# Kernel tuning notes

Measured on AMD Instinct MI355X. Metric: run time of the kernel, lower is better.

## Reference

```python
import jax, jax.numpy as jnp
import numpy as np

STATE_DIM = 32
ACTION_DIM = 8
LATENT_DIM = 64
HIDDEN = 128
X_DIM = ACTION_DIM + 1  # t channel + actions
B = 4096
L = 128
N_SUB = 2  # fixed RK4 substeps per knot interval


def natural_cubic_coeffs(x):
    """Natural cubic spline on unit-spaced knots 0..L-1 (matches torchcde's
    implicit arange grid). x: [B, L, C]. Returns per-interval coeffs b, c, d
    ([B, L-1, C]) s.t. X(i+u) = x_i + b u + c u^2 + d u^3."""
    Bb, Ln, C = x.shape
    n = Ln - 2
    # tridiagonal system for interior second derivatives (natural BC: m0=mL-1=0)
    M = 4.0 * jnp.eye(n, dtype=x.dtype) + jnp.eye(n, k=1, dtype=x.dtype) + jnp.eye(n, k=-1, dtype=x.dtype)
    rhs = 6.0 * (x[:, 2:] - 2.0 * x[:, 1:-1] + x[:, :-2])  # [B, n, C]
    m_in = jnp.linalg.solve(M, rhs.transpose(1, 0, 2).reshape(n, -1))  # [n, B*C]
    m_in = m_in.reshape(n, Bb, C).transpose(1, 0, 2)
    zpad = jnp.zeros((Bb, 1, C), x.dtype)
    m = jnp.concatenate([zpad, m_in, zpad], axis=1)  # [B, L, C]
    b = (x[:, 1:] - x[:, :-1]) - (2.0 * m[:, :-1] + m[:, 1:]) / 6.0
    c = m[:, :-1] / 2.0
    d = (m[:, 1:] - m[:, :-1]) / 6.0
    return b, c, d


def setup_inputs() -> dict:
    key = jax.random.key(0)
    ks = jax.random.split(key, 8)
    s = jax.random.normal(ks[0], (B, L, STATE_DIM), dtype=jnp.float32)
    a = jax.random.normal(ks[1], (B, L, ACTION_DIM), dtype=jnp.float32)
    t = jnp.broadcast_to(jnp.arange(L, dtype=jnp.float32), (B, L)) + jnp.zeros((B, L), jnp.float32)

    def lin(k, fi, fo, scale=1.0):
        return (jax.random.normal(k, (fi, fo), dtype=jnp.float32) * (scale / np.sqrt(fi))).astype(jnp.float32)

    enc_W = lin(ks[2], STATE_DIM + ACTION_DIM + 1, LATENT_DIM)
    enc_b = jnp.zeros((LATENT_DIM,), jnp.float32)
    f_W1 = lin(ks[3], LATENT_DIM, HIDDEN, 0.5)
    f_b1 = jnp.zeros((HIDDEN,), jnp.float32)
    f_W2 = lin(ks[4], HIDDEN, LATENT_DIM * X_DIM, 0.1)  # small scale keeps the CDE stable over 127 time units
    f_b2 = jnp.zeros((LATENT_DIM * X_DIM,), jnp.float32)
    dec_W = lin(ks[5], LATENT_DIM, STATE_DIM)
    dec_b = jnp.zeros((STATE_DIM,), jnp.float32)
    return dict(s=s, a=a, t=t, enc_W=enc_W, enc_b=enc_b, f_W1=f_W1, f_b1=f_b1,
                f_W2=f_W2, f_b2=f_b2, dec_W=dec_W, dec_b=dec_b)


def reference(s, a, t, enc_W, enc_b, f_W1, f_b1, f_W2, f_b2, dec_W, dec_b):
    # control path X = [t, a] : [B, L, X_DIM]
    x = jnp.concatenate([t[..., None], a], axis=-1)
    cb, cc, cd = natural_cubic_coeffs(x)  # each [B, L-1, X_DIM]

    z0 = jnp.concatenate([s[:, 0], a[:, 0], t[:, 0:1]], axis=-1) @ enc_W + enc_b  # [B, latent]

    def vf(z):  # f(z): [B, latent] -> [B, latent, X_DIM]
        h = jax.nn.relu(z @ f_W1 + f_b1)
        return (h @ f_W2 + f_b2).reshape(-1, LATENT_DIM, X_DIM)

    hstep = 1.0 / N_SUB

    def interval(z, coef):
        bi, ci, di = coef  # [B, X_DIM] each, current interval spline coeffs

        def dzdu(z, u):
            dX = bi + 2.0 * ci * u + 3.0 * di * (u * u)  # dX/dt on this interval
            return jnp.einsum('blx,bx->bl', vf(z), dX)

        for k in range(N_SUB):  # small fixed unroll, not a data-dim loop
            u = k * hstep
            k1 = dzdu(z, u)
            k2 = dzdu(z + 0.5 * hstep * k1, u + 0.5 * hstep)
            k3 = dzdu(z + 0.5 * hstep * k2, u + 0.5 * hstep)
            k4 = dzdu(z + hstep * k3, u + hstep)
            z = z + (hstep / 6.0) * (k1 + 2.0 * k2 + 2.0 * k3 + k4)
        return z, z

    coefs = (cb.transpose(1, 0, 2), cc.transpose(1, 0, 2), cd.transpose(1, 0, 2))  # [L-1, B, X_DIM]
    _, zs = jax.lax.scan(interval, z0, coefs)  # zs: [L-1, B, latent]
    z = jnp.concatenate([z0[None], zs], axis=0).transpose(1, 0, 2)  # [B, L, latent]
    return z @ dec_W + dec_b  # [B, L, state_dim]
```

## Files before the change

kernel.cpp:

```cpp
#include <hip/hip_runtime.h>

#define Bsz 4096
#define Lsz 128
#define NI  127
#define SD  32
#define AD  8
#define XDm 9
#define LAT 64
#define HID 128
#define BT  16
#define THR 1024

__global__ __launch_bounds__(256) void repack_w2(const float* __restrict__ W2, float* __restrict__ W2p){
  int idx = blockIdx.x*256 + threadIdx.x;
  if (idx >= HID*LAT*12) return;
  int x = idx % 12; int jl = idx / 12; int l = jl % LAT; int j = jl / LAT;
  W2p[idx] = (x < XDm) ? W2[j*(LAT*XDm) + l*XDm + x] : 0.f;
}

__global__ __launch_bounds__(256) void spline_kernel(const float* __restrict__ t,
                                                     const float* __restrict__ a,
                                                     float* __restrict__ m_ws){
  __shared__ float cp_s[126];
  if (threadIdx.x == 0){
    float c = 0.25f; cp_s[0] = c;
    for (int i=1;i<126;i++){ c = 1.0f/(4.0f - c); cp_s[i] = c; }
  }
  __syncthreads();
  int tid = blockIdx.x*256 + threadIdx.x;
  int b = tid/XDm, c = tid%XDm;
  float dp[126];
  const float* tb = t + (size_t)b*Lsz;
  const float* ab = a + (size_t)b*Lsz*AD + (c-1);
  float x0 = (c==0)? tb[0] : ab[0];
  float x1 = (c==0)? tb[1] : ab[AD];
  for (int i=0;i<126;i++){
    float x2 = (c==0)? tb[i+2] : ab[(size_t)(i+2)*AD];
    float rhs = 6.0f*(x2 - 2.0f*x1 + x0);
    dp[i] = (i==0)? rhs*0.25f : (rhs - dp[i-1])*cp_s[i];
    x0 = x1; x1 = x2;
  }
  m_ws[tid] = 0.0f;
  m_ws[(size_t)127*(Bsz*XDm) + tid] = 0.0f;
  float mn = 0.0f;
  for (int k=125;k>=0;k--){
    mn = dp[k] - cp_s[k]*mn;
    m_ws[(size_t)(k+1)*(Bsz*XDm) + tid] = mn;
  }
}

#define BFLY(MASK_IMM) { _Pragma("unroll") \
  for (int b_=0;b_<16;b_++) \
    dz[b_] += __int_as_float(__builtin_amdgcn_ds_swizzle(__float_as_int(dz[b_]), MASK_IMM)); }

__global__ __launch_bounds__(THR, 4) void cde_integrate(
    const float* __restrict__ s, const float* __restrict__ a, const float* __restrict__ t,
    const float* __restrict__ encW, const float* __restrict__ encb,
    const float* __restrict__ W1, const float* __restrict__ b1,
    const float* __restrict__ b2, const float* __restrict__ decW, const float* __restrict__ decb,
    const float* __restrict__ W2p, const float* __restrict__ m_ws,
    float* __restrict__ out)
{
  __shared__ float W1t[HID][LAT+4];
  __shared__ float hs[BT][HID+4];
  __shared__ float zs[BT][LAT+4];
  __shared__ float dXs[5][BT][12];
  __shared__ float bds[BT][LAT+4];
  __shared__ float dWs[LAT][SD];
  __shared__ float b1s[HID];
  __shared__ float b2s[LAT][12];
  __shared__ float dbs[SD];

  const int tid = threadIdx.x;
  const int b0 = blockIdx.x * BT;

  for (int i=tid;i<HID*LAT;i+=THR){ int j = i & (HID-1); int k = i >> 7; W1t[j][k] = W1[k*HID+j]; }
  for (int i=tid;i<LAT*SD;i+=THR)  ((float*)dWs)[i] = decW[i];
  if (tid < HID) b1s[tid] = b1[tid];
  for (int i=tid;i<LAT*12;i+=THR){ int l=i/12, x=i%12; b2s[l][x] = (x<XDm)? b2[l*XDm+x] : 0.f; }
  if (tid < SD) dbs[tid] = decb[tid];

  const int ol = tid >> 4;
  const int jg = tid & 15;
  float4 wa[8], wb[8]; float wc[8];
  {
    const float4* W2p4 = (const float4*)W2p;
    #pragma unroll
    for (int jj=0;jj<8;jj++){
      size_t base = ((size_t)(jg*8+jj)*LAT + ol)*3;
      wa[jj] = W2p4[base]; wb[jj] = W2p4[base+1]; wc[jj] = W2p[(base+2)*4];
    }
  }

  {
    const int bb = tid >> 6;
    const int li = tid & 63;
    const float* sb = s + (size_t)(b0+bb)*Lsz*SD;
    const float* ab = a + (size_t)(b0+bb)*Lsz*AD;
    const float tv = t[(size_t)(b0+bb)*Lsz];
    float acc = encb[li];
    #pragma unroll
    for (int k=0;k<SD;k++) acc = fmaf(sb[k], encW[k*LAT+li], acc);
    #pragma unroll
    for (int k=0;k<AD;k++) acc = fmaf(ab[k], encW[(SD+k)*LAT+li], acc);
    acc = fmaf(tv, encW[(SD+AD)*LAT+li], acc);
    zs[bb][li] = acc;
  }
  __syncthreads();

  if (tid < BT*SD){
    const int bb = tid >> 5; const int o = tid & 31;
    float acc = dbs[o];
    #pragma unroll 8
    for (int k=0;k<LAT;k++) acc = fmaf(zs[bb][k], dWs[k][o], acc);
    out[((size_t)(b0+bb)*Lsz + 0)*SD + o] = acc;
  }

  float zb = zs[jg][ol];
  float ka = 0.f;

  for (int iv=0; iv<NI; iv++){
    if (tid < 5*BT*XDm){
      int ui = tid/(BT*XDm); int r = tid%(BT*XDm); int bb = r/XDm; int x = r%XDm;
      float u = 0.25f*(float)ui;
      int gb = b0+bb;
      float m0 = m_ws[(size_t)iv    *(Bsz*XDm) + (size_t)gb*XDm + x];
      float m1 = m_ws[(size_t)(iv+1)*(Bsz*XDm) + (size_t)gb*XDm + x];
      float xd;
      if (x==0) xd = t[(size_t)gb*Lsz + iv+1] - t[(size_t)gb*Lsz + iv];
      else      xd = a[((size_t)gb*Lsz + iv+1)*AD + x-1] - a[((size_t)gb*Lsz + iv)*AD + x-1];
      float cb = xd - (2.f*m0 + m1)*(1.f/6.f);
      float cc = 0.5f*m0;
      float cd = (m1 - m0)*(1.f/6.f);
      dXs[ui][bb][x] = cb + (2.f*cc)*u + (3.f*cd)*(u*u);
    }

    for (int st=0; st<8; st++){
      const int ui = (st+1)>>1;
      const int mode = st & 3;
      __syncthreads();

      {
        const int j0 = 2*ol;
        float acc0 = b1s[j0], acc1 = b1s[j0+1];
        const float4* z4 = (const float4*)&zs[jg][0];
        const float4* w0 = (const float4*)&W1t[j0][0];
        const float4* w1 = (const float4*)&W1t[j0+1][0];
        #pragma unroll
        for (int k4=0;k4<LAT/4;k4++){
          float4 zv = z4[k4]; float4 u0 = w0[k4]; float4 u1 = w1[k4];
          acc0 = fmaf(zv.x,u0.x,acc0); acc0 = fmaf(zv.y,u0.y,acc0);
          acc0 = fmaf(zv.z,u0.z,acc0); acc0 = fmaf(zv.w,u0.w,acc0);
          acc1 = fmaf(zv.x,u1.x,acc1); acc1 = fmaf(zv.y,u1.y,acc1);
          acc1 = fmaf(zv.z,u1.z,acc1); acc1 = fmaf(zv.w,u1.w,acc1);
        }
        hs[jg][j0]   = fmaxf(acc0, 0.f);
        hs[jg][j0+1] = fmaxf(acc1, 0.f);
      }
      {
        const int bb = tid >> 6; const int ll = tid & 63;
        float sacc = 0.f;
        #pragma unroll
        for (int x=0;x<XDm;x++) sacc = fmaf(b2s[ll][x], dXs[ui][bb][x], sacc);
        bds[bb][ll] = sacc;
      }
      __syncthreads();

      float dz[16];
      #pragma unroll
      for (int b=0;b<16;b++){
        float4 dxa = *(const float4*)&dXs[ui][b][0];
        float4 dxb = *(const float4*)&dXs[ui][b][4];
        float  dxc = dXs[ui][b][8];
        float4 h0  = *(const float4*)&hs[b][jg*8];
        float4 h1  = *(const float4*)&hs[b][jg*8+4];
        float acc = 0.f;
        #define STEP(JJ, HV) { \
          float wd = fmaf(wa[JJ].x,dxa.x, fmaf(wa[JJ].y,dxa.y, fmaf(wa[JJ].z,dxa.z, fmaf(wa[JJ].w,dxa.w, \
                     fmaf(wb[JJ].x,dxb.x, fmaf(wb[JJ].y,dxb.y, fmaf(wb[JJ].z,dxb.z, fmaf(wb[JJ].w,dxb.w, \
                     wc[JJ]*dxc)))))))); \
          acc = fmaf(HV, wd, acc); }
        STEP(0,h0.x) STEP(1,h0.y) STEP(2,h0.z) STEP(3,h0.w)
        STEP(4,h1.x) STEP(5,h1.y) STEP(6,h1.z) STEP(7,h1.w)
        #undef STEP
        dz[b] = acc;
      }
      BFLY(0x041F) BFLY(0x081F) BFLY(0x101F) BFLY(0x201F)
      float dzm = dz[0];
      #pragma unroll
      for (int b=1;b<16;b++) dzm = (jg==b)? dz[b] : dzm;
      dzm += bds[jg][ol];
      if (mode == 0){        ka = dzm;
        zs[jg][ol] = zb + 0.25f*dzm;
      } else if (mode == 1){ ka = fmaf(2.f, dzm, ka);
        zs[jg][ol] = zb + 0.25f*dzm;
      } else if (mode == 2){ ka = fmaf(2.f, dzm, ka);
        zs[jg][ol] = zb + 0.5f*dzm;
      } else {               ka += dzm;
        zb = fmaf(0.5f/6.f, ka, zb);
        zs[jg][ol] = zb;
      }
    }

    __syncthreads();
    if (tid < BT*SD){
      const int bb = tid >> 5; const int o = tid & 31;
      float acc = dbs[o];
      #pragma unroll 8
      for (int k=0;k<LAT;k++) acc = fmaf(zs[bb][k], dWs[k][o], acc);
      out[((size_t)(b0+bb)*Lsz + (iv+1))*SD + o] = acc;
    }
  }
}

extern "C" void kernel_launch(void* const* d_in, const int* in_sizes, int n_in,
                              void* d_out, int out_size, void* d_ws, size_t ws_size,
                              hipStream_t stream){
  const float* s    = (const float*)d_in[0];
  const float* a    = (const float*)d_in[1];
  const float* t    = (const float*)d_in[2];
  const float* encW = (const float*)d_in[3];
  const float* encb = (const float*)d_in[4];
  const float* W1   = (const float*)d_in[5];
  const float* b1   = (const float*)d_in[6];
  const float* W2   = (const float*)d_in[7];
  const float* b2   = (const float*)d_in[8];
  const float* decW = (const float*)d_in[9];
  const float* decb = (const float*)d_in[10];
  float* out = (float*)d_out;
  float* ws  = (float*)d_ws;
  float* W2p  = ws;
  float* m_ws = ws + HID*LAT*12;

  hipLaunchKernelGGL(repack_w2, dim3((HID*LAT*12+255)/256), dim3(256), 0, stream, W2, W2p);
  hipLaunchKernelGGL(spline_kernel, dim3(Bsz*XDm/256), dim3(256), 0, stream, t, a, m_ws);
  hipLaunchKernelGGL(cde_integrate, dim3(Bsz/BT), dim3(THR), 0, stream,
                     s,a,t,encW,encb,W1,b1,b2,decW,decb,W2p,m_ws,out);
}
```

Measured before the change: 9.637 ms.

## Use transpose-style DPP reduction and padded hidden layout in CDE vector-field step

Replaces the 16-value butterfly all-reduce (64 ds_swizzle ops per step) with a recursive-halving exchange that sends half the partial sums at each level. It uses DPP moves for the xor-1 and xor-2 stages and ds_swizzle only for xor-4 and xor-8, processing the batch in two groups of eight. The hidden activations are stored with a 12-float stride per 8-float group, which is meant to cut LDS bank conflicts on the per-thread float4 reads, and the bias-dX dot product is vectorised. Register pinning via empty asm keeps the W2 weights resident, at the cost of some added register pressure and extra select instructions.

```diff
diff --git a/kernel.cpp b/kernel.cpp
--- a/kernel.cpp
+++ b/kernel.cpp
@@ -49,9 +49,12 @@
   }
 }
 
-#define BFLY(MASK_IMM) { _Pragma("unroll") \
-  for (int b_=0;b_<16;b_++) \
-    dz[b_] += __int_as_float(__builtin_amdgcn_ds_swizzle(__float_as_int(dz[b_]), MASK_IMM)); }
+#define DPP_XOR1(v) __int_as_float(__builtin_amdgcn_mov_dpp(__float_as_int(v), 0xB1, 0xF, 0xF, true))
+#define DPP_XOR2(v) __int_as_float(__builtin_amdgcn_mov_dpp(__float_as_int(v), 0x4E, 0xF, 0xF, true))
+#define SWZ_XOR4(v) __int_as_float(__builtin_amdgcn_ds_swizzle(__float_as_int(v), 0x101F))
+#define SWZ_XOR8(v) __int_as_float(__builtin_amdgcn_ds_swizzle(__float_as_int(v), 0x201F))
+
+#define HROW 196
 
 __global__ __launch_bounds__(THR, 4) void cde_integrate(
     const float* __restrict__ s, const float* __restrict__ a, const float* __restrict__ t,
@@ -62,7 +65,7 @@
     float* __restrict__ out)
 {
   __shared__ float W1t[HID][LAT+4];
-  __shared__ float hs[BT][HID+4];
+  __shared__ float hs[BT][HROW];
   __shared__ float zs[BT][LAT+4];
   __shared__ float dXs[5][BT][12];
   __shared__ float bds[BT][LAT+4];
@@ -80,18 +83,6 @@
   for (int i=tid;i<LAT*12;i+=THR){ int l=i/12, x=i%12; b2s[l][x] = (x<XDm)? b2[l*XDm+x] : 0.f; }
   if (tid < SD) dbs[tid] = decb[tid];
 
-  const int ol = tid >> 4;
-  const int jg = tid & 15;
-  float4 wa[8], wb[8]; float wc[8];
-  {
-    const float4* W2p4 = (const float4*)W2p;
-    #pragma unroll
-    for (int jj=0;jj<8;jj++){
-      size_t base = ((size_t)(jg*8+jj)*LAT + ol)*3;
-      wa[jj] = W2p4[base]; wb[jj] = W2p4[base+1]; wc[jj] = W2p[(base+2)*4];
-    }
-  }
-
   {
     const int bb = tid >> 6;
     const int li = tid & 63;
@@ -114,6 +105,25 @@
     #pragma unroll 8
     for (int k=0;k<LAT;k++) acc = fmaf(zs[bb][k], dWs[k][o], acc);
     out[((size_t)(b0+bb)*Lsz + 0)*SD + o] = acc;
+  }
+
+  const int ol = tid >> 4;
+  const int jg = tid & 15;
+
+  float4 wa[8], wb[8]; float wc[8];
+  {
+    const float4* W2p4 = (const float4*)W2p;
+    #pragma unroll
+    for (int jj=0;jj<8;jj++){
+      size_t base = ((size_t)(jg*8+jj)*LAT + ol)*3;
+      wa[jj] = W2p4[base]; wb[jj] = W2p4[base+1]; wc[jj] = W2p[(base+2)*4];
+    }
+    #pragma unroll
+    for (int jj=0;jj<8;jj++){
+      asm volatile("" : "+v"(wa[jj].x), "+v"(wa[jj].y), "+v"(wa[jj].z), "+v"(wa[jj].w),
+                        "+v"(wb[jj].x), "+v"(wb[jj].y), "+v"(wb[jj].z), "+v"(wb[jj].w),
+                        "+v"(wc[jj]));
+    }
   }
 
   float zb = zs[jg][ol];
@@ -154,42 +164,79 @@
           acc1 = fmaf(zv.x,u1.x,acc1); acc1 = fmaf(zv.y,u1.y,acc1);
           acc1 = fmaf(zv.z,u1.z,acc1); acc1 = fmaf(zv.w,u1.w,acc1);
         }
-        hs[jg][j0]   = fmaxf(acc0, 0.f);
-        hs[jg][j0+1] = fmaxf(acc1, 0.f);
+        float2 hv; hv.x = fmaxf(acc0,0.f); hv.y = fmaxf(acc1,0.f);
+        *(float2*)&hs[jg][(j0>>3)*12 + (j0&7)] = hv;
       }
       {
-        const int bb = tid >> 6; const int ll = tid & 63;
-        float sacc = 0.f;
-        #pragma unroll
-        for (int x=0;x<XDm;x++) sacc = fmaf(b2s[ll][x], dXs[ui][bb][x], sacc);
-        bds[bb][ll] = sacc;
+        const int w = tid >> 6; const int ll = tid & 63;
+        const float4 ba = *(const float4*)&b2s[ll][0];
+        const float4 bb4 = *(const float4*)&b2s[ll][4];
+        const float  bc = b2s[ll][8];
+        const float4 da = *(const float4*)&dXs[ui][w][0];
+        const float4 db = *(const float4*)&dXs[ui][w][4];
+        const float  dc = dXs[ui][w][8];
+        float sacc = bc*dc;
+        sacc = fmaf(ba.x,da.x, fmaf(ba.y,da.y, fmaf(ba.z,da.z, fmaf(ba.w,da.w, sacc))));
+        sacc = fmaf(bb4.x,db.x, fmaf(bb4.y,db.y, fmaf(bb4.z,db.z, fmaf(bb4.w,db.w, sacc))));
+        bds[w][ll] = sacc;
       }
       __syncthreads();
 
-      float dz[16];
-      #pragma unroll
-      for (int b=0;b<16;b++){
-        float4 dxa = *(const float4*)&dXs[ui][b][0];
-        float4 dxb = *(const float4*)&dXs[ui][b][4];
-        float  dxc = dXs[ui][b][8];
-        float4 h0  = *(const float4*)&hs[b][jg*8];
-        float4 h1  = *(const float4*)&hs[b][jg*8+4];
-        float acc = 0.f;
-        #define STEP(JJ, HV) { \
-          float wd = fmaf(wa[JJ].x,dxa.x, fmaf(wa[JJ].y,dxa.y, fmaf(wa[JJ].z,dxa.z, fmaf(wa[JJ].w,dxa.w, \
-                     fmaf(wb[JJ].x,dxb.x, fmaf(wb[JJ].y,dxb.y, fmaf(wb[JJ].z,dxb.z, fmaf(wb[JJ].w,dxb.w, \
-                     wc[JJ]*dxc)))))))); \
-          acc = fmaf(HV, wd, acc); }
-        STEP(0,h0.x) STEP(1,h0.y) STEP(2,h0.z) STEP(3,h0.w)
-        STEP(4,h1.x) STEP(5,h1.y) STEP(6,h1.z) STEP(7,h1.w)
-        #undef STEP
-        dz[b] = acc;
-      }
-      BFLY(0x041F) BFLY(0x081F) BFLY(0x101F) BFLY(0x201F)
-      float dzm = dz[0];
-      #pragma unroll
-      for (int b=1;b<16;b++) dzm = (jg==b)? dz[b] : dzm;
-      dzm += bds[jg][ol];
+      auto gemm2_batch = [&](const int bb0)->float {
+        float dz[8];
+        #pragma unroll
+        for (int i=0;i<8;i++){
+          const int b = bb0 + i;
+          const float4 dxa = *(const float4*)&dXs[ui][b][0];
+          const float4 dxb = *(const float4*)&dXs[ui][b][4];
+          const float  dxc = dXs[ui][b][8];
+          const float4 h0 = *(const float4*)&hs[b][jg*12];
+          const float4 h1 = *(const float4*)&hs[b][jg*12+4];
+          float acc = 0.f;
+          #define STEP(JJ, HV) { \
+            float wd = fmaf(wa[JJ].x,dxa.x, fmaf(wa[JJ].y,dxa.y, fmaf(wa[JJ].z,dxa.z, fmaf(wa[JJ].w,dxa.w, \
+                       fmaf(wb[JJ].x,dxb.x, fmaf(wb[JJ].y,dxb.y, fmaf(wb[JJ].z,dxb.z, fmaf(wb[JJ].w,dxb.w, \
+                       wc[JJ]*dxc)))))))); \
+            acc = fmaf(HV, wd, acc); }
+          STEP(0,h0.x) STEP(1,h0.y) STEP(2,h0.z) STEP(3,h0.w)
+          STEP(4,h1.x) STEP(5,h1.y) STEP(6,h1.z) STEP(7,h1.w)
+          #undef STEP
+          dz[i] = acc;
+        }
+        const bool g1 = (jg&1);
+        float nd[4];
+        #pragma unroll
+        for (int i=0;i<4;i++){
+          float lo = dz[2*i], hi = dz[2*i+1];
+          float send = g1 ? lo : hi;
+          float recv = DPP_XOR1(send);
+          float keep = g1 ? hi : lo;
+          nd[i] = keep + recv;
+        }
+        const bool g2 = (jg&2);
+        float md[2];
+        #pragma unroll
+        for (int i=0;i<2;i++){
+          float lo = nd[2*i], hi = nd[2*i+1];
+          float send = g2 ? lo : hi;
+          float recv = DPP_XOR2(send);
+          float keep = g2 ? hi : lo;
+          md[i] = keep + recv;
+        }
+        const bool g4 = (jg&4);
+        {
+          float lo = md[0], hi = md[1];
+          float send = g4 ? lo : hi;
+          float recv = SWZ_XOR4(send);
+          float keep = g4 ? hi : lo;
+          float r = keep + recv;
+          return r + SWZ_XOR8(r);
+        }
+      };
+      const float totA = gemm2_batch(0);
+      const float totB = gemm2_batch(8);
+      float dzm = ((jg&8)? totB : totA) + bds[jg][ol];
+
       if (mode == 0){        ka = dzm;
         zs[jg][ol] = zb + 0.25f*dzm;
       } else if (mode == 1){ ka = fmaf(2.f, dzm, ka);
```

Result: faster. 9.054 ms (-6.0%).
